# Kernel optimization log

Hardware: AMD Instinct MI355X
Metric: run time of the kernel (lower is better)

Reference implementation:

```python
import jax, jax.numpy as jnp
import numpy as np

DELTA_VAR = 0.5
DELTA_DIST = 1.5
LOSS_WEIGHT = 1.0
L_MAX = 17  # segment ids 0..16 (0 = background)
EPS = 1e-12


def setup_inputs() -> dict:
    key = jax.random.key(0)
    k1, k2 = jax.random.split(key)
    B, D, H, W = 16, 16, 288, 512
    emb = jax.random.normal(k1, (B, D, H, W), dtype=jnp.float32)
    seg = jax.random.randint(k2, (B, 1, H, W), 0, L_MAX, dtype=jnp.int64)
    return {"input": emb, "target": seg}


def _per_image_losses(e, s):
    # e: [D, N] float, s: [N] int labels in [0, L_MAX)
    D, N = e.shape
    et = e.T  # [N, D]
    cnt = jax.ops.segment_sum(jnp.ones((N,), e.dtype), s, num_segments=L_MAX)  # [L]
    sums = jax.ops.segment_sum(et, s, num_segments=L_MAX)                      # [L, D]
    present = (cnt > 0) & (jnp.arange(L_MAX) != 0)
    num_lanes = jnp.sum(present).astype(e.dtype)
    means = sums / jnp.maximum(cnt, 1.0)[:, None]                              # [L, D]

    # variance (pull) term: per-pixel distance to own-label centroid
    diff = et - means[s]                                                       # [N, D]
    nrm = jnp.sqrt(jnp.maximum(jnp.sum(diff * diff, axis=1), EPS))             # [N]
    term = jax.nn.relu(nrm - DELTA_VAR) ** 2
    per_label = jax.ops.segment_sum(term, s, num_segments=L_MAX) / jnp.maximum(cnt, 1.0)
    var_l = jnp.sum(jnp.where(present, per_label, 0.0)) / jnp.maximum(num_lanes, 1.0)
    var_l = jnp.where(num_lanes > 0, var_l, 0.0)

    # distance (push) term: pairwise centroid distances among present lanes
    d = means[:, None, :] - means[None, :, :]                                  # [L, L, D]
    sumsq = jnp.sum(d * d, axis=2)                                             # [L, L]
    pair_mask = present[:, None] & present[None, :] & ~jnp.eye(L_MAX, dtype=bool)
    dist = jnp.sqrt(jnp.where(pair_mask, sumsq, 1.0))
    push = jnp.sum(jnp.where(pair_mask, jax.nn.relu(DELTA_DIST - dist) ** 2, 0.0))
    denom = jnp.maximum(num_lanes * (num_lanes - 1.0), 1.0)
    dist_l = jnp.where(num_lanes > 1, push / denom / 2.0, 0.0)
    return var_l, dist_l


def reference(input, target):
    B, D, H, W = input.shape
    N = H * W
    emb = input.reshape(B, D, N)
    seg = target.reshape(B, N).astype(jnp.int32)
    var_l, dist_l = jax.vmap(_per_image_losses)(emb, seg)
    loss = (jnp.sum(var_l) + jnp.sum(dist_l)) / B
    return loss * LOSS_WEIGHT
```

## Files before the change

kernel.cpp:

```cpp
#include <hip/hip_runtime.h>

#define BB   16
#define DD   16
#define NN   (288*512)
#define LL   17
#define TPB  256
#define NREP 16

#define PB   144
#define QB   (NN/4/PB)
#define PBV  144

#define FSCALE 32768.0f
#define INV_FSCALE (1.0f/32768.0f)


__global__ __launch_bounds__(TPB) void k_accum(const float* __restrict__ emb,
                                               const int* __restrict__ seg,
                                               int* __restrict__ acc) {
    __shared__ int tab[NREP * 289];
    const int tid  = threadIdx.x;
    const int b    = blockIdx.y;
    const int blk  = blockIdx.x;
    const int dgrp = tid >> 6;
    const int j    = tid & 63;
    int* trep = tab + (j & (NREP - 1)) * 289;

    for (int i = tid; i < NREP * 289; i += TPB) tab[i] = 0;

    const float* embb = emb + (size_t)b * DD * NN;
    const int*   segb = seg + (size_t)b * NN;
    const float* r0 = embb + (size_t)(dgrp * 4 + 0) * NN;
    const float* r1 = embb + (size_t)(dgrp * 4 + 1) * NN;
    const float* r2 = embb + (size_t)(dgrp * 4 + 2) * NN;
    const float* r3 = embb + (size_t)(dgrp * 4 + 3) * NN;
    const int q0 = blk * QB;
    __syncthreads();

    int n = (q0 + j) * 4;
    int4   s4 = *(const int4*)(segb + n);
    float4 e0 = *(const float4*)(r0 + n);
    float4 e1 = *(const float4*)(r1 + n);
    float4 e2 = *(const float4*)(r2 + n);
    float4 e3 = *(const float4*)(r3 + n);

#pragma unroll
    for (int it = 0; it < QB / 64; ++it) {
        int4 s4n; float4 e0n, e1n, e2n, e3n;
        if (it + 1 < QB / 64) {
            const int nn_ = (q0 + (it + 1) * 64 + j) * 4;
            s4n = *(const int4*)(segb + nn_);
            e0n = *(const float4*)(r0 + nn_);
            e1n = *(const float4*)(r1 + nn_);
            e2n = *(const float4*)(r2 + nn_);
            e3n = *(const float4*)(r3 + nn_);
        }
        const int ch = dgrp * 4;
        if (s4.x) {
            const int o0 = s4.x * 17 + ch;
            atomicAdd(trep + o0 + 0, __float2int_rn(e0.x * FSCALE));
            atomicAdd(trep + o0 + 1, __float2int_rn(e1.x * FSCALE));
            atomicAdd(trep + o0 + 2, __float2int_rn(e2.x * FSCALE));
            atomicAdd(trep + o0 + 3, __float2int_rn(e3.x * FSCALE));
            if (dgrp == 0) atomicAdd(trep + s4.x * 17 + 16, 1);
        }
        if (s4.y) {
            const int o1 = s4.y * 17 + ch;
            atomicAdd(trep + o1 + 0, __float2int_rn(e0.y * FSCALE));
            atomicAdd(trep + o1 + 1, __float2int_rn(e1.y * FSCALE));
            atomicAdd(trep + o1 + 2, __float2int_rn(e2.y * FSCALE));
            atomicAdd(trep + o1 + 3, __float2int_rn(e3.y * FSCALE));
            if (dgrp == 0) atomicAdd(trep + s4.y * 17 + 16, 1);
        }
        if (s4.z) {
            const int o2 = s4.z * 17 + ch;
            atomicAdd(trep + o2 + 0, __float2int_rn(e0.z * FSCALE));
            atomicAdd(trep + o2 + 1, __float2int_rn(e1.z * FSCALE));
            atomicAdd(trep + o2 + 2, __float2int_rn(e2.z * FSCALE));
            atomicAdd(trep + o2 + 3, __float2int_rn(e3.z * FSCALE));
            if (dgrp == 0) atomicAdd(trep + s4.z * 17 + 16, 1);
        }
        if (s4.w) {
            const int o3 = s4.w * 17 + ch;
            atomicAdd(trep + o3 + 0, __float2int_rn(e0.w * FSCALE));
            atomicAdd(trep + o3 + 1, __float2int_rn(e1.w * FSCALE));
            atomicAdd(trep + o3 + 2, __float2int_rn(e2.w * FSCALE));
            atomicAdd(trep + o3 + 3, __float2int_rn(e3.w * FSCALE));
            if (dgrp == 0) atomicAdd(trep + s4.w * 17 + 16, 1);
        }
        s4 = s4n; e0 = e0n; e1 = e1n; e2 = e2n; e3 = e3n;
    }
    __syncthreads();

    for (int i = tid; i < 289; i += TPB) {
        int v = 0;
#pragma unroll
        for (int r = 0; r < NREP; ++r) v += tab[r * 289 + i];
        atomicAdd(acc + b * 289 + i, v);
    }
}

__global__ __launch_bounds__(TPB, 4) void k_var(const float* __restrict__ emb,
                                                const int* __restrict__ seg,
                                                const int* __restrict__ acc,
                                                float* __restrict__ vpart) {
    __shared__ float m[289];
    __shared__ float wl[17];
    __shared__ float wsum[TPB / 64];
    const int tid = threadIdx.x;
    const int b = blockIdx.y;

    for (int i = tid; i < 289; i += TPB) {
        const int raw = acc[b * 289 + i];
        m[i] = (i % 17 == 16) ? (float)raw : (float)raw * INV_FSCALE;
    }
    __syncthreads();
    for (int i = tid; i < 272; i += TPB) {
        const int l = i >> 4, d = i & 15;
        m[l * 17 + d] /= fmaxf(m[l * 17 + 16], 1.f);
    }
    __syncthreads();

    int nl = 0;
#pragma unroll
    for (int l = 1; l < LL; ++l) nl += (m[l * 17 + 16] > 0.f) ? 1 : 0;
    const float nlf = (float)nl;
    if (tid < LL) {
        const bool pres = (tid != 0) && (m[tid * 17 + 16] > 0.f);
        wl[tid] = pres ? 1.f / (fmaxf(m[tid * 17 + 16], 1.f) * fmaxf(nlf, 1.f) * (float)BB)
                       : 0.f;
    }
    __syncthreads();

    const float* embb = emb + (size_t)b * DD * NN;
    const int*   segb = seg + (size_t)b * NN;

    const int n = blockIdx.x * (TPB * 4) + tid * 4;
    const int4 s4 = *(const int4*)(segb + n);

    float4 e[DD];
#pragma unroll
    for (int d = 0; d < DD; ++d)
        e[d] = *(const float4*)(embb + (size_t)d * NN + n);

    const int o0 = s4.x * 17, o1 = s4.y * 17, o2 = s4.z * 17, o3 = s4.w * 17;
    float ss0 = 0.f, ss1 = 0.f, ss2 = 0.f, ss3 = 0.f;
#pragma unroll
    for (int d = 0; d < DD; ++d) {
        const float d0 = e[d].x - m[o0 + d]; ss0 += d0 * d0;
        const float d1 = e[d].y - m[o1 + d]; ss1 += d1 * d1;
        const float d2 = e[d].z - m[o2 + d]; ss2 += d2 * d2;
        const float d3 = e[d].w - m[o3 + d]; ss3 += d3 * d3;
    }
    float accl = 0.f, t;
    t = fmaxf(sqrtf(fmaxf(ss0, 1e-12f)) - 0.5f, 0.f); accl += t * t * wl[s4.x];
    t = fmaxf(sqrtf(fmaxf(ss1, 1e-12f)) - 0.5f, 0.f); accl += t * t * wl[s4.y];
    t = fmaxf(sqrtf(fmaxf(ss2, 1e-12f)) - 0.5f, 0.f); accl += t * t * wl[s4.z];
    t = fmaxf(sqrtf(fmaxf(ss3, 1e-12f)) - 0.5f, 0.f); accl += t * t * wl[s4.w];

    if (blockIdx.x == 0 && nl > 1) {
        float push = 0.f;
        for (int p = tid; p < 289; p += TPB) {
            const int i = p / 17, jj = p % 17;
            if (i != jj && i > 0 && jj > 0 && m[i*17+16] > 0.f && m[jj*17+16] > 0.f) {
                float ss = 0.f;
#pragma unroll
                for (int d = 0; d < DD; ++d) {
                    const float df = m[i*17+d] - m[jj*17+d];
                    ss += df * df;
                }
                const float u = fmaxf(1.5f - sqrtf(ss), 0.f);
                push += u * u;
            }
        }
        accl += push / (fmaxf(nlf * (nlf - 1.f), 1.f) * 2.f * (float)BB);
    }

#pragma unroll
    for (int off = 32; off; off >>= 1) accl += __shfl_down(accl, off, 64);
    if ((tid & 63) == 0) wsum[tid >> 6] = accl;
    __syncthreads();
    if (tid == 0)
        vpart[(size_t)b * PBV + blockIdx.x] = wsum[0] + wsum[1] + wsum[2] + wsum[3];
}

__global__ __launch_bounds__(TPB) void k_final(const float* __restrict__ vpart,
                                               float* __restrict__ out) {
    __shared__ float ws4[TPB / 64];
    float v = 0.f;
    for (int i = threadIdx.x; i < BB * PBV; i += TPB) v += vpart[i];
#pragma unroll
    for (int off = 32; off; off >>= 1) v += __shfl_down(v, off, 64);
    if ((threadIdx.x & 63) == 0) ws4[threadIdx.x >> 6] = v;
    __syncthreads();
    if (threadIdx.x == 0) out[0] = ws4[0] + ws4[1] + ws4[2] + ws4[3];
}

extern "C" void kernel_launch(void* const* d_in, const int* in_sizes, int n_in,
                              void* d_out, int out_size, void* d_ws, size_t ws_size,
                              hipStream_t stream) {
    const float* emb = (const float*)d_in[0];
    const int*   seg = (const int*)d_in[1];
    float* out = (float*)d_out;

    int*   acc   = (int*)d_ws;
    float* vpart = (float*)(acc + BB * 289);

    hipMemsetAsync(acc, 0, (size_t)BB * 289 * sizeof(int), stream);

    k_accum<<<dim3(PB, BB), TPB, 0, stream>>>(emb, seg, acc);
    k_var  <<<dim3(PBV, BB), TPB, 0, stream>>>(emb, seg, acc, vpart);
    k_final<<<1, TPB, 0, stream>>>(vpart, out);
}
```

Measured before the change: 243.6 us.

## Replace global atomics with per-block partials and hoist means into reduce kernel

```diff
diff --git a/kernel.cpp b/kernel.cpp
--- a/kernel.cpp
+++ b/kernel.cpp
@@ -7,17 +7,18 @@
 #define TPB  256
 #define NREP 16
 
-#define PB   144
+#define PB   48
 #define QB   (NN/4/PB)
 #define PBV  144
 
 #define FSCALE 32768.0f
 #define INV_FSCALE (1.0f/32768.0f)
+#define MW_STRIDE 320
 
 
 __global__ __launch_bounds__(TPB) void k_accum(const float* __restrict__ emb,
                                                const int* __restrict__ seg,
-                                               int* __restrict__ acc) {
+                                               int* __restrict__ part) {
     __shared__ int tab[NREP * 289];
     const int tid  = threadIdx.x;
     const int b    = blockIdx.y;
@@ -92,27 +93,30 @@
     }
     __syncthreads();
 
+    int* pout = part + ((size_t)b * PB + blk) * 289;
     for (int i = tid; i < 289; i += TPB) {
         int v = 0;
 #pragma unroll
         for (int r = 0; r < NREP; ++r) v += tab[r * 289 + i];
-        atomicAdd(acc + b * 289 + i, v);
-    }
-}
-
-__global__ __launch_bounds__(TPB, 4) void k_var(const float* __restrict__ emb,
-                                                const int* __restrict__ seg,
-                                                const int* __restrict__ acc,
+        pout[i] = v;
+    }
+}
+
+__global__ __launch_bounds__(TPB) void k_reduce(const int* __restrict__ part,
+                                                float* __restrict__ mw,
                                                 float* __restrict__ vpart) {
     __shared__ float m[289];
     __shared__ float wl[17];
-    __shared__ float wsum[TPB / 64];
+    __shared__ float psum[TPB / 64];
     const int tid = threadIdx.x;
-    const int b = blockIdx.y;
+    const int b = blockIdx.x;
 
     for (int i = tid; i < 289; i += TPB) {
-        const int raw = acc[b * 289 + i];
-        m[i] = (i % 17 == 16) ? (float)raw : (float)raw * INV_FSCALE;
+        const int* p = part + (size_t)b * PB * 289 + i;
+        int s = 0;
+#pragma unroll 8
+        for (int k = 0; k < PB; ++k) s += p[(size_t)k * 289];
+        m[i] = (i % 17 == 16) ? (float)s : (float)s * INV_FSCALE;
     }
     __syncthreads();
     for (int i = tid; i < 272; i += TPB) {
@@ -132,34 +136,8 @@
     }
     __syncthreads();
 
-    const float* embb = emb + (size_t)b * DD * NN;
-    const int*   segb = seg + (size_t)b * NN;
-
-    const int n = blockIdx.x * (TPB * 4) + tid * 4;
-    const int4 s4 = *(const int4*)(segb + n);
-
-    float4 e[DD];
-#pragma unroll
-    for (int d = 0; d < DD; ++d)
-        e[d] = *(const float4*)(embb + (size_t)d * NN + n);
-
-    const int o0 = s4.x * 17, o1 = s4.y * 17, o2 = s4.z * 17, o3 = s4.w * 17;
-    float ss0 = 0.f, ss1 = 0.f, ss2 = 0.f, ss3 = 0.f;
-#pragma unroll
-    for (int d = 0; d < DD; ++d) {
-        const float d0 = e[d].x - m[o0 + d]; ss0 += d0 * d0;
-        const float d1 = e[d].y - m[o1 + d]; ss1 += d1 * d1;
-        const float d2 = e[d].z - m[o2 + d]; ss2 += d2 * d2;
-        const float d3 = e[d].w - m[o3 + d]; ss3 += d3 * d3;
-    }
-    float accl = 0.f, t;
-    t = fmaxf(sqrtf(fmaxf(ss0, 1e-12f)) - 0.5f, 0.f); accl += t * t * wl[s4.x];
-    t = fmaxf(sqrtf(fmaxf(ss1, 1e-12f)) - 0.5f, 0.f); accl += t * t * wl[s4.y];
-    t = fmaxf(sqrtf(fmaxf(ss2, 1e-12f)) - 0.5f, 0.f); accl += t * t * wl[s4.z];
-    t = fmaxf(sqrtf(fmaxf(ss3, 1e-12f)) - 0.5f, 0.f); accl += t * t * wl[s4.w];
-
-    if (blockIdx.x == 0 && nl > 1) {
-        float push = 0.f;
+    float push = 0.f;
+    if (nl > 1) {
         for (int p = tid; p < 289; p += TPB) {
             const int i = p / 17, jj = p % 17;
             if (i != jj && i > 0 && jj > 0 && m[i*17+16] > 0.f && m[jj*17+16] > 0.f) {
@@ -173,8 +151,58 @@
                 push += u * u;
             }
         }
-        accl += push / (fmaxf(nlf * (nlf - 1.f), 1.f) * 2.f * (float)BB);
-    }
+    }
+#pragma unroll
+    for (int off = 32; off; off >>= 1) push += __shfl_down(push, off, 64);
+    if ((tid & 63) == 0) psum[tid >> 6] = push;
+    __syncthreads();
+    if (tid == 0) {
+        const float tot = psum[0] + psum[1] + psum[2] + psum[3];
+        vpart[(size_t)BB * PBV + b] =
+            (nl > 1) ? tot / (fmaxf(nlf * (nlf - 1.f), 1.f) * 2.f * (float)BB) : 0.f;
+    }
+
+    for (int i = tid; i < 289 + LL; i += TPB)
+        mw[(size_t)b * MW_STRIDE + i] = (i < 289) ? m[i] : wl[i - 289];
+}
+
+__global__ __launch_bounds__(TPB, 4) void k_var(const float* __restrict__ emb,
+                                                const int* __restrict__ seg,
+                                                const float* __restrict__ mw,
+                                                float* __restrict__ vpart) {
+    __shared__ float md[306];
+    __shared__ float wsum[TPB / 64];
+    const int tid = threadIdx.x;
+    const int b = blockIdx.y;
+
+    for (int i = tid; i < 306; i += TPB) md[i] = mw[(size_t)b * MW_STRIDE + i];
+    __syncthreads();
+
+    const float* embb = emb + (size_t)b * DD * NN;
+    const int*   segb = seg + (size_t)b * NN;
+
+    const int n = blockIdx.x * (TPB * 4) + tid * 4;
+    const int4 s4 = *(const int4*)(segb + n);
+
+    float4 e[DD];
+#pragma unroll
+    for (int d = 0; d < DD; ++d)
+        e[d] = *(const float4*)(embb + (size_t)d * NN + n);
+
+    const int o0 = s4.x * 17, o1 = s4.y * 17, o2 = s4.z * 17, o3 = s4.w * 17;
+    float ss0 = 0.f, ss1 = 0.f, ss2 = 0.f, ss3 = 0.f;
+#pragma unroll
+    for (int d = 0; d < DD; ++d) {
+        const float d0 = e[d].x - md[o0 + d]; ss0 += d0 * d0;
+        const float d1 = e[d].y - md[o1 + d]; ss1 += d1 * d1;
+        const float d2 = e[d].z - md[o2 + d]; ss2 += d2 * d2;
+        const float d3 = e[d].w - md[o3 + d]; ss3 += d3 * d3;
+    }
+    float accl = 0.f, t;
+    t = fmaxf(sqrtf(fmaxf(ss0, 1e-12f)) - 0.5f, 0.f); accl += t * t * md[289 + s4.x];
+    t = fmaxf(sqrtf(fmaxf(ss1, 1e-12f)) - 0.5f, 0.f); accl += t * t * md[289 + s4.y];
+    t = fmaxf(sqrtf(fmaxf(ss2, 1e-12f)) - 0.5f, 0.f); accl += t * t * md[289 + s4.z];
+    t = fmaxf(sqrtf(fmaxf(ss3, 1e-12f)) - 0.5f, 0.f); accl += t * t * md[289 + s4.w];
 
 #pragma unroll
     for (int off = 32; off; off >>= 1) accl += __shfl_down(accl, off, 64);
@@ -188,7 +216,7 @@
                                                float* __restrict__ out) {
     __shared__ float ws4[TPB / 64];
     float v = 0.f;
-    for (int i = threadIdx.x; i < BB * PBV; i += TPB) v += vpart[i];
+    for (int i = threadIdx.x; i < BB * PBV + BB; i += TPB) v += vpart[i];
 #pragma unroll
     for (int off = 32; off; off >>= 1) v += __shfl_down(v, off, 64);
     if ((threadIdx.x & 63) == 0) ws4[threadIdx.x >> 6] = v;
@@ -203,12 +231,12 @@
     const int*   seg = (const int*)d_in[1];
     float* out = (float*)d_out;
 
-    int*   acc   = (int*)d_ws;
-    float* vpart = (float*)(acc + BB * 289);
-
-    hipMemsetAsync(acc, 0, (size_t)BB * 289 * sizeof(int), stream);
-
-    k_accum<<<dim3(PB, BB), TPB, 0, stream>>>(emb, seg, acc);
-    k_var  <<<dim3(PBV, BB), TPB, 0, stream>>>(emb, seg, acc, vpart);
-    k_final<<<1, TPB, 0, stream>>>(vpart, out);
-}
+    int*   part  = (int*)d_ws;
+    float* mw    = (float*)(part + (size_t)BB * PB * 289);
+    float* vpart = mw + (size_t)BB * MW_STRIDE;
+
+    k_accum <<<dim3(PB, BB), TPB, 0, stream>>>(emb, seg, part);
+    k_reduce<<<BB, TPB, 0, stream>>>(part, mw, vpart);
+    k_var   <<<dim3(PBV, BB), TPB, 0, stream>>>(emb, seg, mw, vpart);
+    k_final <<<1, TPB, 0, stream>>>(vpart, out);
+}
```

After: 252.9 us. 3.8% more time.
